# Kernel tuning notes

Hardware: AMD Instinct MI355X
Metric: run time of the kernel (lower is better)

Reference implementation:

```python
import jax, jax.numpy as jnp
import numpy as np

B, N, NPOINT, C = 4, 16384, 4096, 64
NSAMPLE = 32


def setup_inputs() -> dict:
    key = jax.random.key(0)
    k1, k2, k3 = jax.random.split(key, 3)
    xyz = jax.random.normal(k1, (B, N, 3), dtype=jnp.float32)
    new_xyz = jax.random.normal(k2, (B, NPOINT, 3), dtype=jnp.float32)
    features = jax.random.normal(k3, (B, C, N), dtype=jnp.float32)
    return {"xyz": xyz, "new_xyz": new_xyz, "features": features, "nsample": NSAMPLE}


def _knn_idx(new_xyz, xyz, k):
    # squared pairwise distances: (B, npoint, N)
    dists = jnp.sum((new_xyz[:, :, None, :] - xyz[:, None, :, :]) ** 2, axis=-1)
    # k smallest distances -> top_k on negated distances (fused top-k instead of full argsort)
    _, idx = jax.lax.top_k(-dists, k)  # (B, npoint, k) int32
    return idx


def reference(xyz, new_xyz, features, nsample):
    idx = _knn_idx(new_xyz, xyz, nsample)  # (B, npoint, nsample)

    # group xyz: (B, npoint, nsample, 3)
    grouped_xyz = jax.vmap(lambda pts, i: pts[i])(xyz, idx)
    # center on the query points and move coords to channel dim: (B, 3, npoint, nsample)
    grouped_xyz = grouped_xyz - new_xyz[:, :, None, :]
    grouped_xyz = jnp.transpose(grouped_xyz, (0, 3, 1, 2))

    # group features: (B, C, npoint, nsample)
    grouped_features = jax.vmap(lambda f, i: f[:, i])(features, idx)

    # use_xyz=True -> concat along channel dim: (B, 3 + C, npoint, nsample)
    new_features = jnp.concatenate([grouped_xyz, grouped_features], axis=1)
    return new_features
```

## Files before the change

kernel.cpp:

```cpp
#include <hip/hip_runtime.h>

#define NBATCH 4
#define NPTS   16384
#define NQ     4096
#define NCH    64
#define K      32
#define CHOUT  67

typedef float v2f __attribute__((ext_vector_type(2)));
typedef float v4f __attribute__((ext_vector_type(4)));
typedef int   v4i __attribute__((ext_vector_type(4)));

__device__ __forceinline__ v2f pk_add(v2f a, v2f b) {
    v2f d; asm("v_pk_add_f32 %0, %1, %2" : "=v"(d) : "v"(a), "v"(b)); return d;
}
__device__ __forceinline__ v2f pk_mul(v2f a, v2f b) {
    v2f d; asm("v_pk_mul_f32 %0, %1, %2" : "=v"(d) : "v"(a), "v"(b)); return d;
}
__device__ __forceinline__ v2f pk_fma(v2f a, v2f b, v2f c) {
    v2f d; asm("v_pk_fma_f32 %0, %1, %2, %3" : "=v"(d) : "v"(a), "v"(b), "v"(c)); return d;
}
__device__ __forceinline__ int dpp_shr1(int v) {
    return __builtin_amdgcn_update_dpp(v, v, 0x138, 0xf, 0xf, false);
}
__device__ __forceinline__ int sel_mask_i(unsigned long long m, int t, int f) {
    int d; asm("v_cndmask_b32 %0, %2, %1, %3" : "=v"(d) : "v"(t), "v"(f), "s"(m));
    return d;
}

constexpr int TILE = 1024;
constexpr int NT   = NPTS / TILE;
constexpr int QPW  = 4;
constexpr int QPB  = 16;

#define VW3 asm volatile("s_waitcnt vmcnt(3)" ::: "memory")
#define VW0 asm volatile("s_waitcnt vmcnt(0)" ::: "memory")
#define BAR __builtin_amdgcn_s_barrier()

template <bool FUSED>
__global__ __launch_bounds__(256) void knn_kernel(
    const float* __restrict__ xyz,
    const float* __restrict__ new_xyz,
    const float* __restrict__ ft,
    int*   __restrict__ out_idx,
    float* __restrict__ out)
{
    __shared__ __align__(16) float sb[3][TILE * 3];

    const int tid  = threadIdx.x;
    const int lane = tid & 63;
    const int wave = tid >> 6;
    const int b    = blockIdx.x >> 8;
    const int q0   = (blockIdx.x & 255) * QPB + wave * QPW;

    const float* xb = xyz + (size_t)b * NPTS * 3;
    const char* gbase = (const char*)xb + wave * 3072 + lane * 16;

    auto STAGE = [&](int buf, int t0) {
        const char* g = gbase + (size_t)t0 * 12;
        char* l = (char*)(&sb[buf][0]) + wave * 3072;
#define GLL(k) __builtin_amdgcn_global_load_lds( \
        (const __attribute__((address_space(1))) unsigned int*)(g + (k) * 1024), \
        (__attribute__((address_space(3))) unsigned int*)(l + (k) * 1024), \
        16, 0, 0)
        GLL(0); GLL(1); GLL(2);
#undef GLL
    };

    float nqx[QPW], nqy[QPW], nqz[QPW];
    v2f nqx2[QPW], nqy2[QPW], nqz2[QPW];
#pragma unroll
    for (int j = 0; j < QPW; ++j) {
        const int base = ((b * NQ) + q0 + j) * 3;
        nqx[j] = __int_as_float(__builtin_amdgcn_readfirstlane(__float_as_int(-new_xyz[base + 0])));
        nqy[j] = __int_as_float(__builtin_amdgcn_readfirstlane(__float_as_int(-new_xyz[base + 1])));
        nqz[j] = __int_as_float(__builtin_amdgcn_readfirstlane(__float_as_int(-new_xyz[base + 2])));
        nqx2[j] = (v2f){nqx[j], nqx[j]};
        nqy2[j] = (v2f){nqy[j], nqy[j]};
        nqz2[j] = (v2f){nqz[j], nqz[j]};
    }

    const float INF  = __int_as_float(0x7f800000);
    const float NINF = __int_as_float(0xff800000);

    float vmA[QPW], vmB[QPW];
#pragma unroll
    for (int j = 0; j < QPW; ++j) { vmA[j] = INF; vmB[j] = INF; }

    STAGE(0, 0);
    STAGE(1, TILE);
    VW3; BAR;
    {
        int cur = 0, pre = 2;
        for (int t = 0; t < NT; ++t) {
            if (t + 2 < NT) STAGE(pre, (t + 2) * TILE);
            const float* sp = &sb[cur][0];
#pragma unroll
            for (int ii = 0; ii < TILE / 128; ++ii) {
                const float* qp = sp + 3 * (ii * 128 + lane);
                const v2f px2 = {qp[0], qp[192]};
                const v2f py2 = {qp[1], qp[193]};
                const v2f pz2 = {qp[2], qp[194]};
#pragma unroll
                for (int j = 0; j < QPW; ++j) {
                    const v2f dx = pk_add(px2, nqx2[j]);
                    const v2f dy = pk_add(py2, nqy2[j]);
                    const v2f dz = pk_add(pz2, nqz2[j]);
                    const v2f d2 = pk_fma(dx, dx, pk_fma(dy, dy, pk_mul(dz, dz)));
                    vmA[j] = fminf(vmA[j], d2.x);
                    vmB[j] = fminf(vmB[j], d2.y);
                }
            }
            if (t + 1 < NT) {
                if (t + 2 < NT) { VW3; } else { VW0; }
                BAR;
            }
            cur = (cur == 2) ? 0 : cur + 1;
            pre = (pre == 2) ? 0 : pre + 1;
        }
    }
    BAR;

    STAGE(0, 0);
    STAGE(1, TILE);

    float Tf[QPW];
#pragma unroll
    for (int j = 0; j < QPW; ++j) {
        const unsigned u = __float_as_uint(fminf(vmA[j], vmB[j]));
        unsigned t = 0x7fffffffu;
        for (int bb = 30; bb >= 0; --bb) {
            const unsigned tt = t ^ (1u << bb);
            const int cnt = __popcll(__ballot(u <= tt));
            if (cnt >= 32) t = tt;
        }
        Tf[j] = __uint_as_float(t + 64);
    }

    float ld[QPW]; int li[QPW];
#pragma unroll
    for (int j = 0; j < QPW; ++j) {
        ld[j] = (lane < K) ? INF : NINF;
        li[j] = 0;
    }

    VW3; BAR;
    {
        int cur = 0, pre = 2;
        for (int t = 0; t < NT; ++t) {
            if (t + 2 < NT) STAGE(pre, (t + 2) * TILE);
            const int t0 = t * TILE;
            const float* sp = &sb[cur][0];
#pragma unroll
            for (int ii = 0; ii < TILE / 128; ++ii) {
                const int gb = t0 + ii * 128;
                const float* qp = sp + 3 * (ii * 128 + lane);
                const v2f px2 = {qp[0], qp[192]};
                const v2f py2 = {qp[1], qp[193]};
                const v2f pz2 = {qp[2], qp[194]};
#pragma unroll
                for (int j = 0; j < QPW; ++j) {
                    const v2f dx = pk_add(px2, nqx2[j]);
                    const v2f dy = pk_add(py2, nqy2[j]);
                    const v2f dz = pk_add(pz2, nqz2[j]);
                    const v2f d2 = pk_add(pk_add(pk_mul(dx, dx), pk_mul(dy, dy)),
                                          pk_mul(dz, dz));
                    unsigned long long m0 = __ballot(d2.x <= Tf[j]);
                    unsigned long long m1 = __ballot(d2.y <= Tf[j]);
                    while (m0 | m1) {
                        const bool lo = (m0 != 0);
                        const unsigned long long mm = lo ? m0 : m1;
                        const int c = (int)__builtin_ctzll(mm);
                        if (lo) m0 &= m0 - 1; else m1 &= m1 - 1;
                        const int b0 = __builtin_amdgcn_readlane(__float_as_int(d2.x), c);
                        const int b1 = __builtin_amdgcn_readlane(__float_as_int(d2.y), c);
                        const float dn = __int_as_float(lo ? b0 : b1);
                        const int cand = gb + (lo ? 0 : 64) + c;
                        const unsigned long long sh = __ballot(ld[j] > dn);
                        const int p = sh ? (int)__builtin_ctzll(sh) : 64;
                        const int sld = dpp_shr1(__float_as_int(ld[j]));
                        const int sli = dpp_shr1(li[j]);
                        const int nld = sel_mask_i(sh, sld, __float_as_int(ld[j]));
                        const int nli = sel_mask_i(sh, sli, li[j]);
                        ld[j] = __int_as_float((lane == p) ? __float_as_int(dn) : nld);
                        li[j] = (lane == p) ? cand : nli;
                    }
                }
            }
            if (t + 1 < NT) {
                if (t + 2 < NT) { VW3; } else { VW0; }
                BAR;
            }
            cur = (cur == 2) ? 0 : cur + 1;
            pre = (pre == 2) ? 0 : pre + 1;
        }
    }

    const size_t plane = (size_t)NQ * K;
#pragma unroll
    for (int j = 0; j < QPW; ++j) {
        const int q = q0 + j;
        if (lane < K) {
            const int idx = li[j];
            const float px = xb[idx * 3 + 0];
            const float py = xb[idx * 3 + 1];
            const float pz = xb[idx * 3 + 2];
            const size_t o = (((size_t)b * CHOUT + 0) * NQ + q) * K + lane;
            out[o]             = __fadd_rn(px, nqx[j]);
            out[o + plane]     = __fadd_rn(py, nqy[j]);
            out[o + 2 * plane] = __fadd_rn(pz, nqz[j]);
        }
        if (FUSED) {
            const int s = lane & 31, h = lane >> 5;
            const int pidx = __shfl(li[j], s);
            const v4f* src = (const v4f*)(ft + ((size_t)b * NPTS + pidx) * NCH) + h * 8;
            v4f r[8];
#pragma unroll
            for (int k2 = 0; k2 < 8; ++k2) r[k2] = src[k2];
            float* ob = out + (((size_t)b * CHOUT + 3) * NQ + q) * K + s;
#pragma unroll
            for (int k2 = 0; k2 < 8; ++k2) {
                const int c0 = h * 32 + k2 * 4;
                ob[(size_t)(c0 + 0) * plane] = r[k2].x;
                ob[(size_t)(c0 + 1) * plane] = r[k2].y;
                ob[(size_t)(c0 + 2) * plane] = r[k2].z;
                ob[(size_t)(c0 + 3) * plane] = r[k2].w;
            }
        } else if (lane < K) {
            out_idx[((size_t)(b * NQ) + q) * K + lane] = li[j];
        }
    }
}

__global__ __launch_bounds__(256) void transpose_kernel(
    const float* __restrict__ f, float* __restrict__ ft)
{
    __shared__ float sm[128][65];
    const int tid = threadIdx.x;
    const int nb  = blockIdx.x & (NPTS / 128 - 1);
    const int b   = blockIdx.x >> 7;
    const int n0  = nb * 128;
    const float* fb = f + (size_t)b * NCH * NPTS;
    const int nn = tid & 127, chh = tid >> 7;
#pragma unroll
    for (int c = 0; c < NCH; c += 2)
        sm[nn][c + chh] = fb[(size_t)(c + chh) * NPTS + n0 + nn];
    __syncthreads();
    float* ftb = ft + ((size_t)b * NPTS + n0) * NCH;
#pragma unroll
    for (int g = 0; g < 32; ++g) {
        const int o = g * 256 + tid;
        ftb[o] = sm[o >> 6][o & 63];
    }
}

__global__ __launch_bounds__(1024) void gather_kernel(
    const float* __restrict__ features,
    const int*   __restrict__ idx,
    float* __restrict__ out)
{
    __shared__ __align__(16) float row[NPTS];

    const int tid  = threadIdx.x;
    const int half = blockIdx.x & 1;
    const int c    = (blockIdx.x >> 1) & 63;
    const int b    = blockIdx.x >> 7;

    const v4f* src = (const v4f*)(features + ((size_t)(b * NCH + c)) * NPTS);
    for (int k2 = tid; k2 < NPTS / 4; k2 += 1024) ((v4f*)row)[k2] = src[k2];
    __syncthreads();

    const size_t hofs = (size_t)half * (NQ * K / 2);
    const v4i* gi = (const v4i*)(idx + (size_t)b * NQ * K + hofs);
    v4f* dst = (v4f*)(out + ((size_t)(b * CHOUT + 3 + c)) * NQ * K + hofs);

    v4i cur = gi[tid];
#pragma unroll
    for (int it = 0; it < 16; ++it) {
        v4i nxt;
        if (it < 15) nxt = gi[tid + (it + 1) * 1024];
        v4f o;
        o.x = row[cur.x]; o.y = row[cur.y]; o.z = row[cur.z]; o.w = row[cur.w];
        dst[tid + it * 1024] = o;
        cur = nxt;
    }
}

extern "C" void kernel_launch(void* const* d_in, const int* in_sizes, int n_in,
                              void* d_out, int out_size, void* d_ws, size_t ws_size,
                              hipStream_t stream) {
    const float* xyz      = (const float*)d_in[0];
    const float* new_xyz  = (const float*)d_in[1];
    const float* features = (const float*)d_in[2];
    float* out = (float*)d_out;

    const size_t ft_bytes = (size_t)NBATCH * NPTS * NCH * sizeof(float);

    if (ws_size >= ft_bytes) {
        float* featT = (float*)d_ws;
        transpose_kernel<<<dim3(NBATCH * (NPTS / 128)), dim3(256), 0, stream>>>(features, featT);
        knn_kernel<true><<<dim3(NBATCH * (NQ / QPB)), dim3(256), 0, stream>>>(
            xyz, new_xyz, featT, nullptr, out);
    } else {
        int* ws_idx = (int*)d_ws;
        knn_kernel<false><<<dim3(NBATCH * (NQ / QPB)), dim3(256), 0, stream>>>(
            xyz, new_xyz, nullptr, ws_idx, out);
        gather_kernel<<<dim3(NBATCH * NCH * 2), dim3(1024), 0, stream>>>(features, ws_idx, out);
    }
}
```

Before: 291.5 us.

## Use SoA xyz with precomputed norms and expanded-distance threshold pass

Adds a pre-pass kernel that writes xyz in structure-of-arrays layout together with each point's squared norm. The threshold pass then computes |p|^2 - 2p·q with three packed FMAs instead of subtract-square-add. The threshold search now handles signed values and adds the query norm plus a small margin. Candidate ordering is adapted to the interleaved pair layout, the tile size is halved, and the features transpose is rewritten to use vector loads and stores. This costs an extra launch and relies on the margin to cover the rounding error of the expanded form.

Result: slower. 345.6 us (+18.6%).

```diff
diff --git a/kernel.cpp b/kernel.cpp
--- a/kernel.cpp
+++ b/kernel.cpp
@@ -28,24 +28,25 @@
     return d;
 }
 
-constexpr int TILE = 1024;
+constexpr int TILE = 512;
 constexpr int NT   = NPTS / TILE;
 constexpr int QPW  = 4;
 constexpr int QPB  = 16;
 
-#define VW3 asm volatile("s_waitcnt vmcnt(3)" ::: "memory")
+#define VW2 asm volatile("s_waitcnt vmcnt(2)" ::: "memory")
 #define VW0 asm volatile("s_waitcnt vmcnt(0)" ::: "memory")
 #define BAR __builtin_amdgcn_s_barrier()
 
 template <bool FUSED>
 __global__ __launch_bounds__(256) void knn_kernel(
+    const float* __restrict__ xn,
     const float* __restrict__ xyz,
     const float* __restrict__ new_xyz,
     const float* __restrict__ ft,
     int*   __restrict__ out_idx,
     float* __restrict__ out)
 {
-    __shared__ __align__(16) float sb[3][TILE * 3];
+    __shared__ __align__(16) float sb[3][4][TILE];
 
     const int tid  = threadIdx.x;
     const int lane = tid & 63;
@@ -53,22 +54,24 @@
     const int b    = blockIdx.x >> 8;
     const int q0   = (blockIdx.x & 255) * QPB + wave * QPW;
 
-    const float* xb = xyz + (size_t)b * NPTS * 3;
-    const char* gbase = (const char*)xb + wave * 3072 + lane * 16;
+    const float* xb  = xyz + (size_t)b * NPTS * 3;
+    const float* xnb = xn + (size_t)b * 4 * NPTS;
+    const char* gbase = (const char*)(xnb + (size_t)wave * NPTS) + lane * 16;
 
     auto STAGE = [&](int buf, int t0) {
-        const char* g = gbase + (size_t)t0 * 12;
-        char* l = (char*)(&sb[buf][0]) + wave * 3072;
+        const char* g = gbase + (size_t)t0 * 4;
+        char* l = (char*)(&sb[buf][wave][0]);
 #define GLL(k) __builtin_amdgcn_global_load_lds( \
         (const __attribute__((address_space(1))) unsigned int*)(g + (k) * 1024), \
         (__attribute__((address_space(3))) unsigned int*)(l + (k) * 1024), \
         16, 0, 0)
-        GLL(0); GLL(1); GLL(2);
+        GLL(0); GLL(1);
 #undef GLL
     };
 
-    float nqx[QPW], nqy[QPW], nqz[QPW];
+    float nqx[QPW], nqy[QPW], nqz[QPW], q2s[QPW];
     v2f nqx2[QPW], nqy2[QPW], nqz2[QPW];
+    v2f m2x2[QPW], m2y2[QPW], m2z2[QPW];
 #pragma unroll
     for (int j = 0; j < QPW; ++j) {
         const int base = ((b * NQ) + q0 + j) * 3;
@@ -78,6 +81,13 @@
         nqx2[j] = (v2f){nqx[j], nqx[j]};
         nqy2[j] = (v2f){nqy[j], nqy[j]};
         nqz2[j] = (v2f){nqz[j], nqz[j]};
+        const float m2x = nqx[j] + nqx[j];
+        const float m2y = nqy[j] + nqy[j];
+        const float m2z = nqz[j] + nqz[j];
+        m2x2[j] = (v2f){m2x, m2x};
+        m2y2[j] = (v2f){m2y, m2y};
+        m2z2[j] = (v2f){m2z, m2z};
+        q2s[j] = nqx[j] * nqx[j] + nqy[j] * nqy[j] + nqz[j] * nqz[j];
     }
 
     const float INF  = __int_as_float(0x7f800000);
@@ -89,30 +99,30 @@
 
     STAGE(0, 0);
     STAGE(1, TILE);
-    VW3; BAR;
+    VW2; BAR;
     {
         int cur = 0, pre = 2;
         for (int t = 0; t < NT; ++t) {
             if (t + 2 < NT) STAGE(pre, (t + 2) * TILE);
-            const float* sp = &sb[cur][0];
+            const float* sp = &sb[cur][0][0];
 #pragma unroll
             for (int ii = 0; ii < TILE / 128; ++ii) {
-                const float* qp = sp + 3 * (ii * 128 + lane);
-                const v2f px2 = {qp[0], qp[192]};
-                const v2f py2 = {qp[1], qp[193]};
-                const v2f pz2 = {qp[2], qp[194]};
+                const float* qp = sp + ii * 128 + 2 * lane;
+                const v2f x2  = *(const v2f*)(qp);
+                const v2f y2  = *(const v2f*)(qp + TILE);
+                const v2f z2  = *(const v2f*)(qp + 2 * TILE);
+                const v2f n22 = *(const v2f*)(qp + 3 * TILE);
 #pragma unroll
                 for (int j = 0; j < QPW; ++j) {
-                    const v2f dx = pk_add(px2, nqx2[j]);
-                    const v2f dy = pk_add(py2, nqy2[j]);
-                    const v2f dz = pk_add(pz2, nqz2[j]);
-                    const v2f d2 = pk_fma(dx, dx, pk_fma(dy, dy, pk_mul(dz, dz)));
-                    vmA[j] = fminf(vmA[j], d2.x);
-                    vmB[j] = fminf(vmB[j], d2.y);
+                    v2f s = pk_fma(z2, m2z2[j], n22);
+                    s = pk_fma(y2, m2y2[j], s);
+                    s = pk_fma(x2, m2x2[j], s);
+                    vmA[j] = fminf(vmA[j], s.x);
+                    vmB[j] = fminf(vmB[j], s.y);
                 }
             }
             if (t + 1 < NT) {
-                if (t + 2 < NT) { VW3; } else { VW0; }
+                if (t + 2 < NT) { VW2; } else { VW0; }
                 BAR;
             }
             cur = (cur == 2) ? 0 : cur + 1;
@@ -127,14 +137,17 @@
     float Tf[QPW];
 #pragma unroll
     for (int j = 0; j < QPW; ++j) {
-        const unsigned u = __float_as_uint(fminf(vmA[j], vmB[j]));
-        unsigned t = 0x7fffffffu;
-        for (int bb = 30; bb >= 0; --bb) {
+        const unsigned bits = __float_as_uint(fminf(vmA[j], vmB[j]));
+        const unsigned u = bits ^ ((((unsigned)(((int)bits) >> 31)) >> 1) | 0x80000000u);
+        unsigned t = 0xFFFFFFFFu;
+        for (int bb = 31; bb >= 0; --bb) {
             const unsigned tt = t ^ (1u << bb);
             const int cnt = __popcll(__ballot(u <= tt));
             if (cnt >= 32) t = tt;
         }
-        Tf[j] = __uint_as_float(t + 64);
+        const unsigned fb2 = (t & 0x80000000u) ? (t ^ 0x80000000u) : ~t;
+        const float Ts = __uint_as_float(fb2);
+        Tf[j] = __fadd_rn(__fadd_rn(Ts, q2s[j]), 0.01f);
     }
 
     float ld[QPW]; int li[QPW];
@@ -144,38 +157,39 @@
         li[j] = 0;
     }
 
-    VW3; BAR;
+    VW2; BAR;
     {
         int cur = 0, pre = 2;
         for (int t = 0; t < NT; ++t) {
             if (t + 2 < NT) STAGE(pre, (t + 2) * TILE);
             const int t0 = t * TILE;
-            const float* sp = &sb[cur][0];
+            const float* sp = &sb[cur][0][0];
 #pragma unroll
             for (int ii = 0; ii < TILE / 128; ++ii) {
                 const int gb = t0 + ii * 128;
-                const float* qp = sp + 3 * (ii * 128 + lane);
-                const v2f px2 = {qp[0], qp[192]};
-                const v2f py2 = {qp[1], qp[193]};
-                const v2f pz2 = {qp[2], qp[194]};
+                const float* qp = sp + ii * 128 + 2 * lane;
+                const v2f x2 = *(const v2f*)(qp);
+                const v2f y2 = *(const v2f*)(qp + TILE);
+                const v2f z2 = *(const v2f*)(qp + 2 * TILE);
 #pragma unroll
                 for (int j = 0; j < QPW; ++j) {
-                    const v2f dx = pk_add(px2, nqx2[j]);
-                    const v2f dy = pk_add(py2, nqy2[j]);
-                    const v2f dz = pk_add(pz2, nqz2[j]);
+                    const v2f dx = pk_add(x2, nqx2[j]);
+                    const v2f dy = pk_add(y2, nqy2[j]);
+                    const v2f dz = pk_add(z2, nqz2[j]);
                     const v2f d2 = pk_add(pk_add(pk_mul(dx, dx), pk_mul(dy, dy)),
                                           pk_mul(dz, dz));
                     unsigned long long m0 = __ballot(d2.x <= Tf[j]);
                     unsigned long long m1 = __ballot(d2.y <= Tf[j]);
                     while (m0 | m1) {
-                        const bool lo = (m0 != 0);
-                        const unsigned long long mm = lo ? m0 : m1;
-                        const int c = (int)__builtin_ctzll(mm);
+                        const int c0 = m0 ? (int)__builtin_ctzll(m0) : 64;
+                        const int c1 = m1 ? (int)__builtin_ctzll(m1) : 64;
+                        const bool lo = c0 <= c1;
+                        const int c = lo ? c0 : c1;
                         if (lo) m0 &= m0 - 1; else m1 &= m1 - 1;
                         const int b0 = __builtin_amdgcn_readlane(__float_as_int(d2.x), c);
                         const int b1 = __builtin_amdgcn_readlane(__float_as_int(d2.y), c);
                         const float dn = __int_as_float(lo ? b0 : b1);
-                        const int cand = gb + (lo ? 0 : 64) + c;
+                        const int cand = gb + 2 * c + (lo ? 0 : 1);
                         const unsigned long long sh = __ballot(ld[j] > dn);
                         const int p = sh ? (int)__builtin_ctzll(sh) : 64;
                         const int sld = dpp_shr1(__float_as_int(ld[j]));
@@ -188,7 +202,7 @@
                 }
             }
             if (t + 1 < NT) {
-                if (t + 2 < NT) { VW3; } else { VW0; }
+                if (t + 2 < NT) { VW2; } else { VW0; }
                 BAR;
             }
             cur = (cur == 2) ? 0 : cur + 1;
@@ -232,25 +246,47 @@
     }
 }
 
+__global__ __launch_bounds__(256) void xyzn_kernel(
+    const float* __restrict__ xyz, float* __restrict__ xn)
+{
+    const int g = blockIdx.x * 256 + threadIdx.x;
+    const int b = g >> 14, n = g & (NPTS - 1);
+    const float x = xyz[(size_t)g * 3 + 0];
+    const float y = xyz[(size_t)g * 3 + 1];
+    const float z = xyz[(size_t)g * 3 + 2];
+    float* o = xn + (size_t)b * 4 * NPTS + n;
+    o[0]            = x;
+    o[NPTS]         = y;
+    o[2 * NPTS]     = z;
+    o[3 * NPTS]     = __fmaf_rn(z, z, __fmaf_rn(y, y, x * x));
+}
+
 __global__ __launch_bounds__(256) void transpose_kernel(
     const float* __restrict__ f, float* __restrict__ ft)
 {
-    __shared__ float sm[128][65];
+    __shared__ float sm[64][65];
     const int tid = threadIdx.x;
-    const int nb  = blockIdx.x & (NPTS / 128 - 1);
-    const int b   = blockIdx.x >> 7;
-    const int n0  = nb * 128;
+    const int nb  = blockIdx.x & 255;
+    const int b   = blockIdx.x >> 8;
+    const int n0  = nb * 64;
+    const int w = tid >> 6, lane = tid & 63;
+    const int r = lane >> 4, i = lane & 15;
     const float* fb = f + (size_t)b * NCH * NPTS;
-    const int nn = tid & 127, chh = tid >> 7;
-#pragma unroll
-    for (int c = 0; c < NCH; c += 2)
-        sm[nn][c + chh] = fb[(size_t)(c + chh) * NPTS + n0 + nn];
+#pragma unroll
+    for (int g = 0; g < 4; ++g) {
+        const int c = g * 16 + w * 4 + r;
+        const v4f v = *(const v4f*)(fb + (size_t)c * NPTS + n0 + 4 * i);
+        sm[4 * i + 0][c] = v.x;
+        sm[4 * i + 1][c] = v.y;
+        sm[4 * i + 2][c] = v.z;
+        sm[4 * i + 3][c] = v.w;
+    }
     __syncthreads();
     float* ftb = ft + ((size_t)b * NPTS + n0) * NCH;
 #pragma unroll
-    for (int g = 0; g < 32; ++g) {
-        const int o = g * 256 + tid;
-        ftb[o] = sm[o >> 6][o & 63];
+    for (int h = 0; h < 4; ++h) {
+        const int n = h * 16 + w * 4 + r;
+        *(v4f*)(ftb + (size_t)n * NCH + 4 * i) = *(const v4f*)(&sm[n][4 * i]);
     }
 }
 
@@ -294,17 +330,23 @@
     const float* features = (const float*)d_in[2];
     float* out = (float*)d_out;
 
-    const size_t ft_bytes = (size_t)NBATCH * NPTS * NCH * sizeof(float);
-
-    if (ws_size >= ft_bytes) {
+    const size_t ft_bytes  = (size_t)NBATCH * NPTS * NCH * sizeof(float);
+    const size_t xn_bytes  = (size_t)NBATCH * 4 * NPTS * sizeof(float);
+    const size_t idx_bytes = (size_t)NBATCH * NQ * K * sizeof(int);
+
+    if (ws_size >= ft_bytes + xn_bytes) {
         float* featT = (float*)d_ws;
-        transpose_kernel<<<dim3(NBATCH * (NPTS / 128)), dim3(256), 0, stream>>>(features, featT);
+        float* xn    = (float*)((char*)d_ws + ft_bytes);
+        xyzn_kernel<<<dim3(NBATCH * NPTS / 256), dim3(256), 0, stream>>>(xyz, xn);
+        transpose_kernel<<<dim3(NBATCH * (NPTS / 64)), dim3(256), 0, stream>>>(features, featT);
         knn_kernel<true><<<dim3(NBATCH * (NQ / QPB)), dim3(256), 0, stream>>>(
-            xyz, new_xyz, featT, nullptr, out);
+            xn, xyz, new_xyz, featT, nullptr, out);
     } else {
-        int* ws_idx = (int*)d_ws;
+        int*   ws_idx = (int*)d_ws;
+        float* xn     = (float*)((char*)d_ws + idx_bytes);
+        xyzn_kernel<<<dim3(NBATCH * NPTS / 256), dim3(256), 0, stream>>>(xyz, xn);
         knn_kernel<false><<<dim3(NBATCH * (NQ / QPB)), dim3(256), 0, stream>>>(
-            xyz, new_xyz, nullptr, ws_idx, out);
+            xn, xyz, new_xyz, nullptr, ws_idx, out);
         gather_kernel<<<dim3(NBATCH * NCH * 2), dim3(1024), 0, stream>>>(features, ws_idx, out);
     }
 }
```

## Fuse feature transpose into KNN kernel via atomic work-stealing tiles

Applied to the files above, without the earlier changes.

Removes the separate transpose kernel and has KNN blocks grab transpose tiles from a global atomic counter, one before the KNN search and the rest afterward. Before gathering features, each block spins until every tile is done. The aim is to hide the transpose behind KNN compute and save a kernel launch. The transpose itself now uses vectorized loads and an XOR-swizzled LDS layout. The cost is an extra memset, atomic contention, and a spin-wait that relies on all blocks being able to make forward progress.

Result: slower. 448.0 us (+53.7%).

```diff
diff --git a/kernel.cpp b/kernel.cpp
--- a/kernel.cpp
+++ b/kernel.cpp
@@ -32,26 +32,71 @@
 constexpr int NT   = NPTS / TILE;
 constexpr int QPW  = 4;
 constexpr int QPB  = 16;
+constexpr int TTILES = NBATCH * (NPTS / 64);
 
 #define VW3 asm volatile("s_waitcnt vmcnt(3)" ::: "memory")
 #define VW0 asm volatile("s_waitcnt vmcnt(0)" ::: "memory")
 #define BAR __builtin_amdgcn_s_barrier()
+
+__device__ __forceinline__ void do_tile(const float* __restrict__ f,
+                                        float* __restrict__ ft,
+                                        int t, int tid, float (*sm)[64]) {
+    const int nb = t & 255;
+    const int b  = t >> 8;
+    const int n0 = nb * 64;
+    const int w = tid >> 6, lane = tid & 63;
+    const int r = lane >> 4, i = lane & 15;
+    const float* fb = f + (size_t)b * NCH * NPTS;
+#pragma unroll
+    for (int g = 0; g < 4; ++g) {
+        const int c = g * 16 + w * 4 + r;
+        const v4f v = *(const v4f*)(fb + (size_t)c * NPTS + n0 + 4 * i);
+        const int cs = c ^ (i << 2);
+        sm[4 * i + 0][cs] = v.x;
+        sm[4 * i + 1][cs] = v.y;
+        sm[4 * i + 2][cs] = v.z;
+        sm[4 * i + 3][cs] = v.w;
+    }
+    __syncthreads();
+    float* ftb = ft + ((size_t)b * NPTS + n0) * NCH;
+#pragma unroll
+    for (int h = 0; h < 4; ++h) {
+        const int n = h * 16 + w * 4 + r;
+        const int cs = (4 * i) ^ (((n >> 2) & 15) << 2);
+        const v4f v = *(const v4f*)(&sm[n][cs]);
+        *(v4f*)(ftb + (size_t)n * NCH + 4 * i) = v;
+    }
+}
 
 template <bool FUSED>
 __global__ __launch_bounds__(256) void knn_kernel(
     const float* __restrict__ xyz,
     const float* __restrict__ new_xyz,
-    const float* __restrict__ ft,
+    const float* __restrict__ features,
+    float* __restrict__ ft,
+    int*   __restrict__ ctr,
     int*   __restrict__ out_idx,
     float* __restrict__ out)
 {
     __shared__ __align__(16) float sb[3][TILE * 3];
+    __shared__ int s_comm;
 
     const int tid  = threadIdx.x;
     const int lane = tid & 63;
     const int wave = tid >> 6;
     const int b    = blockIdx.x >> 8;
     const int q0   = (blockIdx.x & 255) * QPB + wave * QPW;
+
+    if (FUSED) {
+        if (tid == 0) s_comm = atomicAdd(&ctr[0], 1);
+        __syncthreads();
+        const int t2 = s_comm;
+        if (t2 < TTILES) {
+            do_tile(features, ft, t2, tid, (float(*)[64])&sb[0][0]);
+            __syncthreads();
+            if (tid == 0) { __threadfence(); atomicAdd(&ctr[1], 1); }
+        }
+    }
 
     const float* xb = xyz + (size_t)b * NPTS * 3;
     const char* gbase = (const char*)xb + wave * 3072 + lane * 16;
@@ -210,7 +255,35 @@
             out[o + plane]     = __fadd_rn(py, nqy[j]);
             out[o + 2 * plane] = __fadd_rn(pz, nqz[j]);
         }
-        if (FUSED) {
+        if (!FUSED && lane < K) {
+            out_idx[((size_t)(b * NQ) + q) * K + lane] = li[j];
+        }
+    }
+
+    if (FUSED) {
+        for (;;) {
+            if (tid == 0) {
+                const int d = __hip_atomic_load(&ctr[1], __ATOMIC_RELAXED,
+                                                __HIP_MEMORY_SCOPE_AGENT);
+                s_comm = (d >= TTILES) ? -1 : atomicAdd(&ctr[0], 1);
+            }
+            __syncthreads();
+            const int t2 = s_comm;
+            if (t2 < 0) break;
+            if (t2 < TTILES) {
+                do_tile(features, ft, t2, tid, (float(*)[64])&sb[0][0]);
+                __syncthreads();
+                if (tid == 0) { __threadfence(); atomicAdd(&ctr[1], 1); }
+            } else {
+                __builtin_amdgcn_s_sleep(8);
+            }
+            __syncthreads();
+        }
+        __threadfence();
+
+#pragma unroll
+        for (int j = 0; j < QPW; ++j) {
+            const int q = q0 + j;
             const int s = lane & 31, h = lane >> 5;
             const int pidx = __shfl(li[j], s);
             const v4f* src = (const v4f*)(ft + ((size_t)b * NPTS + pidx) * NCH) + h * 8;
@@ -226,31 +299,7 @@
                 ob[(size_t)(c0 + 2) * plane] = r[k2].z;
                 ob[(size_t)(c0 + 3) * plane] = r[k2].w;
             }
-        } else if (lane < K) {
-            out_idx[((size_t)(b * NQ) + q) * K + lane] = li[j];
-        }
-    }
-}
-
-__global__ __launch_bounds__(256) void transpose_kernel(
-    const float* __restrict__ f, float* __restrict__ ft)
-{
-    __shared__ float sm[128][65];
-    const int tid = threadIdx.x;
-    const int nb  = blockIdx.x & (NPTS / 128 - 1);
-    const int b   = blockIdx.x >> 7;
-    const int n0  = nb * 128;
-    const float* fb = f + (size_t)b * NCH * NPTS;
-    const int nn = tid & 127, chh = tid >> 7;
-#pragma unroll
-    for (int c = 0; c < NCH; c += 2)
-        sm[nn][c + chh] = fb[(size_t)(c + chh) * NPTS + n0 + nn];
-    __syncthreads();
-    float* ftb = ft + ((size_t)b * NPTS + n0) * NCH;
-#pragma unroll
-    for (int g = 0; g < 32; ++g) {
-        const int o = g * 256 + tid;
-        ftb[o] = sm[o >> 6][o & 63];
+        }
     }
 }
 
@@ -294,17 +343,19 @@
     const float* features = (const float*)d_in[2];
     float* out = (float*)d_out;
 
-    const size_t ft_bytes = (size_t)NBATCH * NPTS * NCH * sizeof(float);
-
-    if (ws_size >= ft_bytes) {
+    const size_t ft_bytes  = (size_t)NBATCH * NPTS * NCH * sizeof(float);
+    const size_t idx_bytes = (size_t)NBATCH * NQ * K * sizeof(int);
+
+    if (ws_size >= ft_bytes + 16) {
         float* featT = (float*)d_ws;
-        transpose_kernel<<<dim3(NBATCH * (NPTS / 128)), dim3(256), 0, stream>>>(features, featT);
+        int*   ctr   = (int*)((char*)d_ws + ft_bytes);
+        hipMemsetAsync(ctr, 0, 8, stream);
         knn_kernel<true><<<dim3(NBATCH * (NQ / QPB)), dim3(256), 0, stream>>>(
-            xyz, new_xyz, featT, nullptr, out);
+            xyz, new_xyz, features, featT, ctr, nullptr, out);
     } else {
         int* ws_idx = (int*)d_ws;
         knn_kernel<false><<<dim3(NBATCH * (NQ / QPB)), dim3(256), 0, stream>>>(
-            xyz, new_xyz, nullptr, ws_idx, out);
+            xyz, new_xyz, nullptr, nullptr, nullptr, ws_idx, out);
         gather_kernel<<<dim3(NBATCH * NCH * 2), dim3(1024), 0, stream>>>(features, ws_idx, out);
     }
 }
```

## Use single-wave KNN blocks without barriers and vectorize feature transpose

Applied to the files above, without the earlier changes.

The KNN kernel goes from 256-thread blocks (4 waves sharing an LDS tile) to one-wave blocks, each staging its own 256-point tiles. This removes every workgroup barrier, so each wave's triple-buffered pipeline runs on its own without waiting for slower waves. The cost is that every wave now loads xyz into LDS by itself, which multiplies global and LDS traffic by four. The transpose kernel is also changed to 64-point tiles with float4 loads and stores.

New measurement: 297.1 us. No clear change (+1.9%).

```diff
diff --git a/kernel.cpp b/kernel.cpp
--- a/kernel.cpp
+++ b/kernel.cpp
@@ -28,17 +28,15 @@
     return d;
 }
 
-constexpr int TILE = 1024;
+constexpr int TILE = 256;
 constexpr int NT   = NPTS / TILE;
 constexpr int QPW  = 4;
-constexpr int QPB  = 16;
 
 #define VW3 asm volatile("s_waitcnt vmcnt(3)" ::: "memory")
 #define VW0 asm volatile("s_waitcnt vmcnt(0)" ::: "memory")
-#define BAR __builtin_amdgcn_s_barrier()
 
 template <bool FUSED>
-__global__ __launch_bounds__(256) void knn_kernel(
+__global__ __launch_bounds__(64) void knn_kernel(
     const float* __restrict__ xyz,
     const float* __restrict__ new_xyz,
     const float* __restrict__ ft,
@@ -47,18 +45,16 @@
 {
     __shared__ __align__(16) float sb[3][TILE * 3];
 
-    const int tid  = threadIdx.x;
-    const int lane = tid & 63;
-    const int wave = tid >> 6;
-    const int b    = blockIdx.x >> 8;
-    const int q0   = (blockIdx.x & 255) * QPB + wave * QPW;
+    const int lane = threadIdx.x;
+    const int b    = blockIdx.x >> 10;
+    const int q0   = (blockIdx.x & 1023) * QPW;
 
     const float* xb = xyz + (size_t)b * NPTS * 3;
-    const char* gbase = (const char*)xb + wave * 3072 + lane * 16;
+    const char* gbase = (const char*)xb + lane * 16;
 
     auto STAGE = [&](int buf, int t0) {
         const char* g = gbase + (size_t)t0 * 12;
-        char* l = (char*)(&sb[buf][0]) + wave * 3072;
+        char* l = (char*)(&sb[buf][0]);
 #define GLL(k) __builtin_amdgcn_global_load_lds( \
         (const __attribute__((address_space(1))) unsigned int*)(g + (k) * 1024), \
         (__attribute__((address_space(3))) unsigned int*)(l + (k) * 1024), \
@@ -89,7 +85,7 @@
 
     STAGE(0, 0);
     STAGE(1, TILE);
-    VW3; BAR;
+    VW3;
     {
         int cur = 0, pre = 2;
         for (int t = 0; t < NT; ++t) {
@@ -113,13 +109,11 @@
             }
             if (t + 1 < NT) {
                 if (t + 2 < NT) { VW3; } else { VW0; }
-                BAR;
             }
             cur = (cur == 2) ? 0 : cur + 1;
             pre = (pre == 2) ? 0 : pre + 1;
         }
     }
-    BAR;
 
     STAGE(0, 0);
     STAGE(1, TILE);
@@ -144,7 +138,7 @@
         li[j] = 0;
     }
 
-    VW3; BAR;
+    VW3;
     {
         int cur = 0, pre = 2;
         for (int t = 0; t < NT; ++t) {
@@ -189,7 +183,6 @@
             }
             if (t + 1 < NT) {
                 if (t + 2 < NT) { VW3; } else { VW0; }
-                BAR;
             }
             cur = (cur == 2) ? 0 : cur + 1;
             pre = (pre == 2) ? 0 : pre + 1;
@@ -235,22 +228,29 @@
 __global__ __launch_bounds__(256) void transpose_kernel(
     const float* __restrict__ f, float* __restrict__ ft)
 {
-    __shared__ float sm[128][65];
+    __shared__ float sm[64][65];
     const int tid = threadIdx.x;
-    const int nb  = blockIdx.x & (NPTS / 128 - 1);
-    const int b   = blockIdx.x >> 7;
-    const int n0  = nb * 128;
+    const int nb  = blockIdx.x & 255;
+    const int b   = blockIdx.x >> 8;
+    const int n0  = nb * 64;
+    const int w = tid >> 6, lane = tid & 63;
+    const int r = lane >> 4, i = lane & 15;
     const float* fb = f + (size_t)b * NCH * NPTS;
-    const int nn = tid & 127, chh = tid >> 7;
-#pragma unroll
-    for (int c = 0; c < NCH; c += 2)
-        sm[nn][c + chh] = fb[(size_t)(c + chh) * NPTS + n0 + nn];
+#pragma unroll
+    for (int g = 0; g < 4; ++g) {
+        const int c = g * 16 + w * 4 + r;
+        const v4f v = *(const v4f*)(fb + (size_t)c * NPTS + n0 + 4 * i);
+        sm[4 * i + 0][c] = v.x;
+        sm[4 * i + 1][c] = v.y;
+        sm[4 * i + 2][c] = v.z;
+        sm[4 * i + 3][c] = v.w;
+    }
     __syncthreads();
     float* ftb = ft + ((size_t)b * NPTS + n0) * NCH;
 #pragma unroll
-    for (int g = 0; g < 32; ++g) {
-        const int o = g * 256 + tid;
-        ftb[o] = sm[o >> 6][o & 63];
+    for (int h = 0; h < 4; ++h) {
+        const int n = h * 16 + w * 4 + r;
+        *(v4f*)(ftb + (size_t)n * NCH + 4 * i) = *(const v4f*)(&sm[n][4 * i]);
     }
 }
 
@@ -298,12 +298,12 @@
 
     if (ws_size >= ft_bytes) {
         float* featT = (float*)d_ws;
-        transpose_kernel<<<dim3(NBATCH * (NPTS / 128)), dim3(256), 0, stream>>>(features, featT);
-        knn_kernel<true><<<dim3(NBATCH * (NQ / QPB)), dim3(256), 0, stream>>>(
+        transpose_kernel<<<dim3(NBATCH * (NPTS / 64)), dim3(256), 0, stream>>>(features, featT);
+        knn_kernel<true><<<dim3(NBATCH * (NQ / QPW)), dim3(64), 0, stream>>>(
             xyz, new_xyz, featT, nullptr, out);
     } else {
         int* ws_idx = (int*)d_ws;
-        knn_kernel<false><<<dim3(NBATCH * (NQ / QPB)), dim3(256), 0, stream>>>(
+        knn_kernel<false><<<dim3(NBATCH * (NQ / QPW)), dim3(64), 0, stream>>>(
             xyz, new_xyz, nullptr, ws_idx, out);
         gather_kernel<<<dim3(NBATCH * NCH * 2), dim3(1024), 0, stream>>>(features, ws_idx, out);
     }
```
